# Optimization experiments

Measured on AMD Instinct MI355X. Metric: run time of the kernel, lower is better.

## Reference

```python
import jax, jax.numpy as jnp
import numpy as np

WINDOW = 8
NUM_HEADS = 4


def setup_inputs() -> dict:
    key = jax.random.key(0)
    ks = jax.random.split(key, 5)
    B, T, C = 32, 4096, 256
    s_qkv = (C) ** -0.5
    s_proj = (C) ** -0.5
    return {
        "x": jax.random.normal(ks[0], (B, T, C), dtype=jnp.float32),
        "w_qkv": jax.random.normal(ks[1], (3 * C, C), dtype=jnp.float32) * s_qkv,
        "b_qkv": jax.random.normal(ks[2], (3 * C,), dtype=jnp.float32) * 0.02,
        "w_proj": jax.random.normal(ks[3], (C, C), dtype=jnp.float32) * s_proj,
        "b_proj": jax.random.normal(ks[4], (C,), dtype=jnp.float32) * 0.02,
    }


def reference(x, w_qkv, b_qkv, w_proj, b_proj):
    # Windowed causal self-attention. Dropout is identity (eval mode).
    B_, T_, C = x.shape
    W, H = WINDOW, NUM_HEADS
    hd = C // H
    scale = hd ** -0.5

    xw = x.reshape(-1, W, C)                      # [nW, W, C]
    qkv = xw @ w_qkv.T + b_qkv                    # [nW, W, 3C]
    qkv = qkv.reshape(-1, W, 3, H, hd)
    qkv = jnp.transpose(qkv, (2, 0, 3, 1, 4))     # [3, nW, H, W, hd]
    q, k, v = qkv[0], qkv[1], qkv[2]

    att = jnp.einsum("bhqd,bhkd->bhqk", q, k) * scale  # [nW, H, W, W]
    causal = jnp.tril(jnp.ones((W, W), dtype=bool))
    att = jnp.where(causal, att, jnp.finfo(att.dtype).min)
    att = jax.nn.softmax(att, axis=-1)

    out = jnp.einsum("bhqk,bhkd->bhqd", att, v)   # [nW, H, W, hd]
    out = jnp.transpose(out, (0, 2, 1, 3)).reshape(-1, W, C)
    out = out @ w_proj.T + b_proj                 # [nW, W, C]
    return out.reshape(B_, T_, C)
```

## Files before the change

### kernel.cpp

```cpp
#include <hip/hip_runtime.h>


typedef __attribute__((ext_vector_type(8))) short short8;
typedef __attribute__((ext_vector_type(4))) short short4v;
typedef __attribute__((ext_vector_type(4))) float float4v;

__device__ inline unsigned cvtpk_bf16(float a, float b) {
  unsigned r;
  asm("v_cvt_pk_bf16_f32 %0, %1, %2" : "=v"(r) : "v"(a), "v"(b));
  return r;
}

__global__ void __launch_bounds__(256) wconv_kernel(const float* __restrict__ wqkv,
                                                    const float* __restrict__ wproj,
                                                    short* __restrict__ dst) {
  int i = blockIdx.x * 256 + threadIdx.x;
  float4 v;
  if (i < 49152) v = reinterpret_cast<const float4*>(wqkv)[i];
  else           v = reinterpret_cast<const float4*>(wproj)[i - 49152];
  reinterpret_cast<uint2*>(dst)[i] =
      make_uint2(cvtpk_bf16(v.x, v.y), cvtpk_bf16(v.z, v.w));
}

__global__ void __launch_bounds__(256, 4) attn_kernel(
    const float* __restrict__ x,
    const short* __restrict__ wbf,
    const float* __restrict__ b_qkv,
    const float* __restrict__ b_proj,
    float* __restrict__ out) {

  __shared__ short sA[32 * 264];
  __shared__ short sQK[2 * 32 * 72];
  __shared__ short sVT[64 * 72];
  __shared__ short sP[2 * 16 * 24];

  const int tid  = threadIdx.x;
  const int wv   = tid >> 6;
  const int lane = tid & 63;
  const int L    = lane & 15;
  const int quad = lane >> 4;
  const int bid  = blockIdx.x;
  const bool selw = (((lane >> 5) ^ (lane >> 3)) & 1);

  const float4v fzero = {0.f, 0.f, 0.f, 0.f};

  const float* xg = x + (size_t)bid * (32 * 256);
  #pragma unroll
  for (int i = 0; i < 8; ++i) {
    int idx = i * 1024 + tid * 4;
    float4 v = *reinterpret_cast<const float4*>(xg + idx);
    int row = idx >> 8;
    int col = idx & 255;
    *reinterpret_cast<uint2*>(&sA[row * 264 + col]) =
        make_uint2(cvtpk_bf16(v.x, v.y), cvtpk_bf16(v.z, v.w));
  }
  __syncthreads();

  float oreg[4][16];

  #pragma unroll
  for (int h = 0; h < 4; ++h) {
    float4v acc[2][3];
    #pragma unroll
    for (int rt = 0; rt < 2; ++rt)
      #pragma unroll
      for (int ct = 0; ct < 3; ++ct) acc[rt][ct] = fzero;

    const short* wb[3];
    int s_[3], d0_[3];
    #pragma unroll
    for (int ct = 0; ct < 3; ++ct) {
      int c0 = wv * 48 + ct * 16;
      int s  = c0 >> 6;
      int d0 = c0 & 63;
      s_[ct] = s; d0_[ct] = d0;
      int wrow0 = s * 256 + h * 64 + d0;
      wb[ct] = wbf + (size_t)(wrow0 + L) * 256 + quad * 8;
    }

    #pragma unroll
    for (int kk = 0; kk < 8; ++kk) {
      short8 a[2];
      #pragma unroll
      for (int rt = 0; rt < 2; ++rt)
        a[rt] = *reinterpret_cast<const short8*>(&sA[(rt * 16 + L) * 264 + kk * 32 + quad * 8]);
      short8 b[3];
      #pragma unroll
      for (int ct = 0; ct < 3; ++ct)
        b[ct] = *reinterpret_cast<const short8*>(wb[ct] + kk * 32);
      #pragma unroll
      for (int rt = 0; rt < 2; ++rt)
        #pragma unroll
        for (int ct = 0; ct < 3; ++ct)
          acc[rt][ct] = __builtin_amdgcn_mfma_f32_16x16x32_bf16(a[rt], b[ct], acc[rt][ct], 0, 0, 0);
    }

    #pragma unroll
    for (int ct = 0; ct < 3; ++ct) {
      int s = s_[ct], d0 = d0_[ct];
      float bias = b_qkv[s * 256 + h * 64 + d0 + L];
      #pragma unroll
      for (int rt = 0; rt < 2; ++rt) {
        int row0 = rt * 16 + quad * 4;
        float4v v = acc[rt][ct];
        unsigned u01 = cvtpk_bf16(v[0] + bias, v[1] + bias);
        unsigned u23 = cvtpk_bf16(v[2] + bias, v[3] + bias);
        if (s < 2) {
          short* dq = &sQK[s * (32 * 72) + row0 * 72 + d0 + L];
          dq[0]   = (short)u01;
          dq[72]  = (short)(u01 >> 16);
          dq[144] = (short)u23;
          dq[216] = (short)(u23 >> 16);
        } else {
          *reinterpret_cast<uint2*>(&sVT[(d0 + L) * 72 + row0]) =
              make_uint2(u01, u23);
        }
      }
    }
    __syncthreads();

    if (wv < 2) {
      float4v sacc = fzero;
      #pragma unroll
      for (int ks = 0; ks < 2; ++ks) {
        short8 qa = *reinterpret_cast<const short8*>(&sQK[(wv * 16 + L) * 72 + ks * 32 + quad * 8]);
        short8 kb = *reinterpret_cast<const short8*>(&sQK[32 * 72 + (wv * 16 + L) * 72 + ks * 32 + quad * 8]);
        sacc = __builtin_amdgcn_mfma_f32_16x16x32_bf16(kb, qa, sacc, 0, 0, 0);
      }

      float sv[4];
      #pragma unroll
      for (int r = 0; r < 4; ++r) {
        int kidx = quad * 4 + r;
        bool valid = ((kidx >> 3) == (L >> 3)) && ((kidx & 7) <= (L & 7));
        sv[r] = valid ? sacc[r] * 0.125f : -1e30f;
      }
      float mx = fmaxf(fmaxf(sv[0], sv[1]), fmaxf(sv[2], sv[3]));
      mx = fmaxf(mx, __shfl_xor(mx, 16));
      {
        float mo = __shfl_xor(mx, 32);
        if (selw) mx = mo;
      }
      float e[4];
      float sum = 0.f;
      #pragma unroll
      for (int r = 0; r < 4; ++r) { e[r] = __expf(sv[r] - mx); sum += e[r]; }
      sum += __shfl_xor(sum, 16);
      {
        float so = __shfl_xor(sum, 32);
        if (selw) sum = so;
      }
      float rs = __builtin_amdgcn_rcpf(sum);
      short* sPw = &sP[wv * (16 * 24)];
      *reinterpret_cast<uint2*>(&sPw[L * 24 + quad * 4]) =
          make_uint2(cvtpk_bf16(e[0] * rs, e[1] * rs), cvtpk_bf16(e[2] * rs, e[3] * rs));

      short8 pa = {0, 0, 0, 0, 0, 0, 0, 0};
      if (quad < 2) pa = *reinterpret_cast<const short8*>(&sPw[L * 24 + quad * 8]);
      #pragma unroll
      for (int dc = 0; dc < 4; ++dc) {
        short8 vb = *reinterpret_cast<const short8*>(
            &sVT[(dc * 16 + L) * 72 + wv * 16 + (quad & 1) * 8]);
        float4v o = __builtin_amdgcn_mfma_f32_16x16x32_bf16(pa, vb, fzero, 0, 0, 0);
        #pragma unroll
        for (int r = 0; r < 4; ++r) oreg[h][dc * 4 + r] = o[r];
      }
    }
    if (h != 3) __syncthreads();
  }

  if (wv < 2) {
    #pragma unroll
    for (int h = 0; h < 4; ++h)
      #pragma unroll
      for (int dc = 0; dc < 4; ++dc) {
        unsigned u01 = cvtpk_bf16(oreg[h][dc * 4 + 0], oreg[h][dc * 4 + 1]);
        unsigned u23 = cvtpk_bf16(oreg[h][dc * 4 + 2], oreg[h][dc * 4 + 3]);
        short* dq = &sA[(wv * 16 + quad * 4) * 264 + h * 64 + dc * 16 + L];
        dq[0]       = (short)u01;
        dq[264]     = (short)(u01 >> 16);
        dq[528]     = (short)u23;
        dq[792]     = (short)(u23 >> 16);
      }
  }
  __syncthreads();

  float4v pacc[2][4];
  #pragma unroll
  for (int rt = 0; rt < 2; ++rt)
    #pragma unroll
    for (int ct = 0; ct < 4; ++ct) pacc[rt][ct] = fzero;

  const short* wp = wbf + 768 * 256;
  const short* wpb[4];
  #pragma unroll
  for (int ct = 0; ct < 4; ++ct)
    wpb[ct] = wp + (size_t)(wv * 64 + ct * 16 + L) * 256 + quad * 8;

  #pragma unroll
  for (int kk = 0; kk < 8; ++kk) {
    short8 a[2];
    #pragma unroll
    for (int rt = 0; rt < 2; ++rt)
      a[rt] = *reinterpret_cast<const short8*>(&sA[(rt * 16 + L) * 264 + kk * 32 + quad * 8]);
    short8 b[4];
    #pragma unroll
    for (int ct = 0; ct < 4; ++ct)
      b[ct] = *reinterpret_cast<const short8*>(wpb[ct] + kk * 32);
    #pragma unroll
    for (int rt = 0; rt < 2; ++rt)
      #pragma unroll
      for (int ct = 0; ct < 4; ++ct)
        pacc[rt][ct] = __builtin_amdgcn_mfma_f32_16x16x32_bf16(a[rt], b[ct], pacc[rt][ct], 0, 0, 0);
  }

  float* og = out + (size_t)bid * (32 * 256);
  #pragma unroll
  for (int ct = 0; ct < 4; ++ct) {
    float bias = b_proj[wv * 64 + ct * 16 + L];
    #pragma unroll
    for (int rt = 0; rt < 2; ++rt)
      #pragma unroll
      for (int r = 0; r < 4; ++r)
        og[(rt * 16 + quad * 4 + r) * 256 + wv * 64 + ct * 16 + L] = pacc[rt][ct][r] + bias;
  }
}

extern "C" void kernel_launch(void* const* d_in, const int* in_sizes, int n_in,
                              void* d_out, int out_size, void* d_ws, size_t ws_size,
                              hipStream_t stream) {
  const float* x      = (const float*)d_in[0];
  const float* w_qkv  = (const float*)d_in[1];
  const float* b_qkv  = (const float*)d_in[2];
  const float* w_proj = (const float*)d_in[3];
  const float* b_proj = (const float*)d_in[4];
  float* out = (float*)d_out;
  short* wbf = (short*)d_ws;

  wconv_kernel<<<256, 256, 0, stream>>>(w_qkv, w_proj, wbf);
  attn_kernel<<<4096, 256, 0, stream>>>(x, wbf, b_qkv, b_proj, out);
}
```

Baseline: 438.6 us.

## Assign one head per wave to remove per-head block barriers

Each wave now owns one attention head. It computes that head's full Q, K and V projection and runs the attention for all 32 rows itself, where before the waves split the QKV columns and only two waves did attention. This drops the four per-head __syncthreads and the idle waves during attention. Shared buffers are replicated per head and V^T is repacked with a narrower stride. The cost is higher LDS use, so the launch bound falls from 4 to 2 blocks per SM, which may reduce occupancy.

```diff
diff --git a/kernel.cpp b/kernel.cpp
--- a/kernel.cpp
+++ b/kernel.cpp
@@ -2,7 +2,6 @@
 
 
 typedef __attribute__((ext_vector_type(8))) short short8;
-typedef __attribute__((ext_vector_type(4))) short short4v;
 typedef __attribute__((ext_vector_type(4))) float float4v;
 
 __device__ inline unsigned cvtpk_bf16(float a, float b) {
@@ -22,7 +21,7 @@
       make_uint2(cvtpk_bf16(v.x, v.y), cvtpk_bf16(v.z, v.w));
 }
 
-__global__ void __launch_bounds__(256, 4) attn_kernel(
+__global__ void __launch_bounds__(256, 2) attn_kernel(
     const float* __restrict__ x,
     const short* __restrict__ wbf,
     const float* __restrict__ b_qkv,
@@ -30,12 +29,12 @@
     float* __restrict__ out) {
 
   __shared__ short sA[32 * 264];
-  __shared__ short sQK[2 * 32 * 72];
-  __shared__ short sVT[64 * 72];
-  __shared__ short sP[2 * 16 * 24];
+  __shared__ short sQK[4][2][32 * 72];
+  __shared__ short sVT[4][64 * 40];
+  __shared__ short sP[4][16 * 24];
 
   const int tid  = threadIdx.x;
-  const int wv   = tid >> 6;
+  const int h    = tid >> 6;
   const int lane = tid & 63;
   const int L    = lane & 15;
   const int quad = lane >> 4;
@@ -56,27 +55,15 @@
   }
   __syncthreads();
 
-  float oreg[4][16];
-
-  #pragma unroll
-  for (int h = 0; h < 4; ++h) {
-    float4v acc[2][3];
-    #pragma unroll
-    for (int rt = 0; rt < 2; ++rt)
-      #pragma unroll
-      for (int ct = 0; ct < 3; ++ct) acc[rt][ct] = fzero;
-
-    const short* wb[3];
-    int s_[3], d0_[3];
-    #pragma unroll
-    for (int ct = 0; ct < 3; ++ct) {
-      int c0 = wv * 48 + ct * 16;
-      int s  = c0 >> 6;
-      int d0 = c0 & 63;
-      s_[ct] = s; d0_[ct] = d0;
-      int wrow0 = s * 256 + h * 64 + d0;
-      wb[ct] = wbf + (size_t)(wrow0 + L) * 256 + quad * 8;
-    }
+  #pragma unroll
+  for (int s = 0; s < 3; ++s) {
+    float4v acc[2][4];
+    #pragma unroll
+    for (int rt = 0; rt < 2; ++rt)
+      #pragma unroll
+      for (int ct = 0; ct < 4; ++ct) acc[rt][ct] = fzero;
+
+    const short* wbase = wbf + (size_t)(s * 256 + h * 64 + L) * 256 + quad * 8;
 
     #pragma unroll
     for (int kk = 0; kk < 8; ++kk) {
@@ -84,20 +71,20 @@
       #pragma unroll
       for (int rt = 0; rt < 2; ++rt)
         a[rt] = *reinterpret_cast<const short8*>(&sA[(rt * 16 + L) * 264 + kk * 32 + quad * 8]);
-      short8 b[3];
-      #pragma unroll
-      for (int ct = 0; ct < 3; ++ct)
-        b[ct] = *reinterpret_cast<const short8*>(wb[ct] + kk * 32);
+      short8 b[4];
+      #pragma unroll
+      for (int ct = 0; ct < 4; ++ct)
+        b[ct] = *reinterpret_cast<const short8*>(wbase + ct * 16 * 256 + kk * 32);
       #pragma unroll
       for (int rt = 0; rt < 2; ++rt)
         #pragma unroll
-        for (int ct = 0; ct < 3; ++ct)
+        for (int ct = 0; ct < 4; ++ct)
           acc[rt][ct] = __builtin_amdgcn_mfma_f32_16x16x32_bf16(a[rt], b[ct], acc[rt][ct], 0, 0, 0);
     }
 
     #pragma unroll
-    for (int ct = 0; ct < 3; ++ct) {
-      int s = s_[ct], d0 = d0_[ct];
+    for (int ct = 0; ct < 4; ++ct) {
+      int d0 = ct * 16;
       float bias = b_qkv[s * 256 + h * 64 + d0 + L];
       #pragma unroll
       for (int rt = 0; rt < 2; ++rt) {
@@ -106,83 +93,86 @@
         unsigned u01 = cvtpk_bf16(v[0] + bias, v[1] + bias);
         unsigned u23 = cvtpk_bf16(v[2] + bias, v[3] + bias);
         if (s < 2) {
-          short* dq = &sQK[s * (32 * 72) + row0 * 72 + d0 + L];
+          short* dq = &sQK[h][s][row0 * 72 + d0 + L];
           dq[0]   = (short)u01;
           dq[72]  = (short)(u01 >> 16);
           dq[144] = (short)u23;
           dq[216] = (short)(u23 >> 16);
         } else {
-          *reinterpret_cast<uint2*>(&sVT[(d0 + L) * 72 + row0]) =
+          *reinterpret_cast<uint2*>(&sVT[h][(d0 + L) * 40 + row0]) =
               make_uint2(u01, u23);
         }
       }
     }
-    __syncthreads();
-
-    if (wv < 2) {
-      float4v sacc = fzero;
-      #pragma unroll
-      for (int ks = 0; ks < 2; ++ks) {
-        short8 qa = *reinterpret_cast<const short8*>(&sQK[(wv * 16 + L) * 72 + ks * 32 + quad * 8]);
-        short8 kb = *reinterpret_cast<const short8*>(&sQK[32 * 72 + (wv * 16 + L) * 72 + ks * 32 + quad * 8]);
-        sacc = __builtin_amdgcn_mfma_f32_16x16x32_bf16(kb, qa, sacc, 0, 0, 0);
-      }
-
-      float sv[4];
-      #pragma unroll
-      for (int r = 0; r < 4; ++r) {
-        int kidx = quad * 4 + r;
-        bool valid = ((kidx >> 3) == (L >> 3)) && ((kidx & 7) <= (L & 7));
-        sv[r] = valid ? sacc[r] * 0.125f : -1e30f;
-      }
-      float mx = fmaxf(fmaxf(sv[0], sv[1]), fmaxf(sv[2], sv[3]));
-      mx = fmaxf(mx, __shfl_xor(mx, 16));
-      {
-        float mo = __shfl_xor(mx, 32);
-        if (selw) mx = mo;
-      }
-      float e[4];
-      float sum = 0.f;
-      #pragma unroll
-      for (int r = 0; r < 4; ++r) { e[r] = __expf(sv[r] - mx); sum += e[r]; }
-      sum += __shfl_xor(sum, 16);
-      {
-        float so = __shfl_xor(sum, 32);
-        if (selw) sum = so;
-      }
-      float rs = __builtin_amdgcn_rcpf(sum);
-      short* sPw = &sP[wv * (16 * 24)];
-      *reinterpret_cast<uint2*>(&sPw[L * 24 + quad * 4]) =
-          make_uint2(cvtpk_bf16(e[0] * rs, e[1] * rs), cvtpk_bf16(e[2] * rs, e[3] * rs));
-
-      short8 pa = {0, 0, 0, 0, 0, 0, 0, 0};
-      if (quad < 2) pa = *reinterpret_cast<const short8*>(&sPw[L * 24 + quad * 8]);
-      #pragma unroll
-      for (int dc = 0; dc < 4; ++dc) {
-        short8 vb = *reinterpret_cast<const short8*>(
-            &sVT[(dc * 16 + L) * 72 + wv * 16 + (quad & 1) * 8]);
-        float4v o = __builtin_amdgcn_mfma_f32_16x16x32_bf16(pa, vb, fzero, 0, 0, 0);
-        #pragma unroll
-        for (int r = 0; r < 4; ++r) oreg[h][dc * 4 + r] = o[r];
-      }
-    }
-    if (h != 3) __syncthreads();
-  }
-
-  if (wv < 2) {
-    #pragma unroll
-    for (int h = 0; h < 4; ++h)
-      #pragma unroll
-      for (int dc = 0; dc < 4; ++dc) {
-        unsigned u01 = cvtpk_bf16(oreg[h][dc * 4 + 0], oreg[h][dc * 4 + 1]);
-        unsigned u23 = cvtpk_bf16(oreg[h][dc * 4 + 2], oreg[h][dc * 4 + 3]);
-        short* dq = &sA[(wv * 16 + quad * 4) * 264 + h * 64 + dc * 16 + L];
-        dq[0]       = (short)u01;
-        dq[264]     = (short)(u01 >> 16);
-        dq[528]     = (short)u23;
-        dq[792]     = (short)(u23 >> 16);
-      }
-  }
+  }
+
+  asm volatile("s_waitcnt lgkmcnt(0)" ::: "memory");
+
+  float oreg[2][16];
+  #pragma unroll
+  for (int grp = 0; grp < 2; ++grp) {
+    const int tb = grp * 16;
+    float4v sacc = fzero;
+    #pragma unroll
+    for (int ks = 0; ks < 2; ++ks) {
+      short8 qa = *reinterpret_cast<const short8*>(&sQK[h][0][(tb + L) * 72 + ks * 32 + quad * 8]);
+      short8 kb = *reinterpret_cast<const short8*>(&sQK[h][1][(tb + L) * 72 + ks * 32 + quad * 8]);
+      sacc = __builtin_amdgcn_mfma_f32_16x16x32_bf16(kb, qa, sacc, 0, 0, 0);
+    }
+
+    float sv[4];
+    #pragma unroll
+    for (int r = 0; r < 4; ++r) {
+      int kidx = quad * 4 + r;
+      bool valid = ((kidx >> 3) == (L >> 3)) && ((kidx & 7) <= (L & 7));
+      sv[r] = valid ? sacc[r] * 0.125f : -1e30f;
+    }
+    float mx = fmaxf(fmaxf(sv[0], sv[1]), fmaxf(sv[2], sv[3]));
+    mx = fmaxf(mx, __shfl_xor(mx, 16));
+    {
+      float mo = __shfl_xor(mx, 32);
+      if (selw) mx = mo;
+    }
+    float e[4];
+    float sum = 0.f;
+    #pragma unroll
+    for (int r = 0; r < 4; ++r) { e[r] = __expf(sv[r] - mx); sum += e[r]; }
+    sum += __shfl_xor(sum, 16);
+    {
+      float so = __shfl_xor(sum, 32);
+      if (selw) sum = so;
+    }
+    float rs = __builtin_amdgcn_rcpf(sum);
+    short* sPw = &sP[h][0];
+    *reinterpret_cast<uint2*>(&sPw[L * 24 + quad * 4]) =
+        make_uint2(cvtpk_bf16(e[0] * rs, e[1] * rs), cvtpk_bf16(e[2] * rs, e[3] * rs));
+
+    short8 pa = {0, 0, 0, 0, 0, 0, 0, 0};
+    if (quad < 2) pa = *reinterpret_cast<const short8*>(&sPw[L * 24 + quad * 8]);
+    #pragma unroll
+    for (int dc = 0; dc < 4; ++dc) {
+      short8 vb = *reinterpret_cast<const short8*>(
+          &sVT[h][(dc * 16 + L) * 40 + tb + (quad & 1) * 8]);
+      float4v o = __builtin_amdgcn_mfma_f32_16x16x32_bf16(pa, vb, fzero, 0, 0, 0);
+      #pragma unroll
+      for (int r = 0; r < 4; ++r) oreg[grp][dc * 4 + r] = o[r];
+    }
+  }
+
+  __syncthreads();
+
+  #pragma unroll
+  for (int grp = 0; grp < 2; ++grp)
+    #pragma unroll
+    for (int dc = 0; dc < 4; ++dc) {
+      unsigned u01 = cvtpk_bf16(oreg[grp][dc * 4 + 0], oreg[grp][dc * 4 + 1]);
+      unsigned u23 = cvtpk_bf16(oreg[grp][dc * 4 + 2], oreg[grp][dc * 4 + 3]);
+      short* dq = &sA[(grp * 16 + quad * 4) * 264 + h * 64 + dc * 16 + L];
+      dq[0]       = (short)u01;
+      dq[264]     = (short)(u01 >> 16);
+      dq[528]     = (short)u23;
+      dq[792]     = (short)(u23 >> 16);
+    }
   __syncthreads();
 
   float4v pacc[2][4];
@@ -195,7 +185,7 @@
   const short* wpb[4];
   #pragma unroll
   for (int ct = 0; ct < 4; ++ct)
-    wpb[ct] = wp + (size_t)(wv * 64 + ct * 16 + L) * 256 + quad * 8;
+    wpb[ct] = wp + (size_t)(h * 64 + ct * 16 + L) * 256 + quad * 8;
 
   #pragma unroll
   for (int kk = 0; kk < 8; ++kk) {
@@ -217,12 +207,12 @@
   float* og = out + (size_t)bid * (32 * 256);
   #pragma unroll
   for (int ct = 0; ct < 4; ++ct) {
-    float bias = b_proj[wv * 64 + ct * 16 + L];
+    float bias = b_proj[h * 64 + ct * 16 + L];
     #pragma unroll
     for (int rt = 0; rt < 2; ++rt)
       #pragma unroll
       for (int r = 0; r < 4; ++r)
-        og[(rt * 16 + quad * 4 + r) * 256 + wv * 64 + ct * 16 + L] = pacc[rt][ct][r] + bias;
+        og[(rt * 16 + quad * 4 + r) * 256 + h * 64 + ct * 16 + L] = pacc[rt][ct][r] + bias;
   }
 }
 
```

Measured after the change: 427.1 us. 1.03x faster.
